# Kernel tuning notes

Measured on AMD Instinct MI355X. Metric: run time of the kernel, lower is better.

Reference implementation:

```python
import jax, jax.numpy as jnp
import numpy as np

TOPK_RATIO = 0.1
THRESHOLD = 0.25
OUT_DIM = 256
STATS_DIM = 18
NEG = -1e30  # sentinel for invalid pixels when sorting (values are probs in [0,1])


def setup_inputs() -> dict:
    key = jax.random.key(0)
    k1, k2, k3, k4, k5, k6, k7 = jax.random.split(key, 7)
    B, C, H, W = 16, 4, 512, 512
    evidence_logits = jax.random.normal(k1, (B, C, H, W), dtype=jnp.float32)
    severity_map = jax.random.normal(k2, (B, 1, H, W), dtype=jnp.float32)
    target_mask = jax.random.uniform(k3, (B, 1, H, W), dtype=jnp.float32)
    # LayerNorm(18) params (torch defaults: weight=1, bias=0)
    ln_w = jnp.ones((STATS_DIM,), jnp.float32)
    ln_b = jnp.zeros((STATS_DIM,), jnp.float32)
    # Linear(18, out_dim) and Linear(out_dim, out_dim)
    w1 = jax.random.normal(k4, (STATS_DIM, OUT_DIM), dtype=jnp.float32) * 0.1
    b1 = jax.random.normal(k5, (OUT_DIM,), dtype=jnp.float32) * 0.01
    w2 = jax.random.normal(k6, (OUT_DIM, OUT_DIM), dtype=jnp.float32) * 0.05
    b2 = jax.random.normal(k7, (OUT_DIM,), dtype=jnp.float32) * 0.01
    return {"evidence_logits": evidence_logits, "severity_map": severity_map,
            "target_mask": target_mask, "ln_w": ln_w, "ln_b": ln_b,
            "w1": w1, "b1": b1, "w2": w2, "b2": b2}


def _forward(evidence_logits, severity_map, target_mask, ln_w, ln_b, w1, b1, w2, b2):
    B, C, H, W = evidence_logits.shape
    N = H * W
    prob = jax.nn.softmax(evidence_logits, axis=1).reshape(B, C, N).transpose(0, 2, 1)  # [B,N,4]
    sev = jax.nn.sigmoid(severity_map).reshape(B, N)                                    # [B,N]
    # mask is same spatial size as logits, so nearest resize is identity
    valid = target_mask.reshape(B, N) > 0.5                                             # [B,N] bool
    validf = valid.astype(prob.dtype)
    total = validf.sum(axis=-1)                                                         # [B]
    has = total > 0
    safe_total = jnp.maximum(total, 1.0)
    # k = max(1, round(total * ratio)); total>=1 implies k<=total
    k = jnp.maximum(1, jnp.round(total * TOPK_RATIO)).astype(jnp.int32)                 # [B]

    # per-class masked mean / max
    class_mean = jnp.einsum('bnc,bn->bc', prob, validf) / safe_total[:, None]           # [B,4]
    class_max = jnp.max(jnp.where(valid[:, :, None], prob, NEG), axis=1)                # [B,4]
    class_max = jnp.where(has[:, None], class_max, 0.0)

    # top-k means for 4 class channels + severity at once: sort desc, cumsum, gather at k-1
    vals = jnp.concatenate([prob, sev[:, :, None]], axis=-1)                            # [B,N,5]
    masked = jnp.where(valid[:, :, None], vals, NEG)
    sorted_desc = jnp.sort(masked, axis=1)[:, ::-1, :]                                  # [B,N,5]
    csum = jnp.cumsum(sorted_desc, axis=1)
    idx = (k - 1).astype(jnp.int32)[:, None, None]                                      # [B,1,1]
    topk_mean = jnp.take_along_axis(csum, jnp.broadcast_to(idx, (B, 1, 5)), axis=1)[:, 0, :]
    topk_mean = topk_mean / k[:, None].astype(prob.dtype)                               # [B,5]
    topk_mean = jnp.where(has[:, None], topk_mean, 0.0)
    class_topk = topk_mean[:, :4]                                                       # [B,4]
    sev_topk = topk_mean[:, 4:5]                                                        # [B,1]

    sev_mean = jnp.where(has, jnp.sum(sev * validf, axis=-1) / safe_total, 0.0)[:, None]
    sev_max = jnp.where(has, jnp.max(jnp.where(valid, sev, NEG), axis=-1), 0.0)[:, None]

    damaged_ind = (prob[:, :, 1] + prob[:, :, 2] + prob[:, :, 3] > THRESHOLD).astype(prob.dtype)
    high_ind = (prob[:, :, 2] + prob[:, :, 3] > THRESHOLD).astype(prob.dtype)
    damaged = jnp.where(has, jnp.sum(damaged_ind * validf, axis=-1) / safe_total, 0.0)   # [B]
    high = jnp.where(has, jnp.sum(high_ind * validf, axis=-1) / safe_total, 0.0)         # [B]
    tar = jnp.where(has, validf.mean(axis=-1), 0.0)                                      # [B]

    stats = jnp.concatenate([class_mean, class_max, class_topk,
                             sev_mean, sev_max, sev_topk,
                             damaged[:, None], high[:, None], tar[:, None]], axis=-1)    # [B,18]

    # LayerNorm(18), eps=1e-5
    mu = stats.mean(axis=-1, keepdims=True)
    var = jnp.mean((stats - mu) ** 2, axis=-1, keepdims=True)
    normed = (stats - mu) * jax.lax.rsqrt(var + 1e-5) * ln_w + ln_b
    h1 = jax.nn.gelu(normed @ w1 + b1, approximate=False)
    projected = h1 @ w2 + b2                                                             # [B,256]
    return stats, projected, damaged, high, tar


def reference(evidence_logits, severity_map, target_mask, ln_w, ln_b, w1, b1, w2, b2):
    return _forward(evidence_logits, severity_map, target_mask, ln_w, ln_b, w1, b1, w2, b2)
```

## Files before the change

### kernel.cpp

```cpp
#include <hip/hip_runtime.h>
#include <math.h>

#define NB 512
#define CHN 5

static constexpr int kN = 512 * 512;
static constexpr int kB = 16;
static constexpr int kChunks = 32;
static constexpr int kThreads1 = 1024;
static constexpr int kPixPerBlock = kN / kChunks;
static constexpr int kF4PerBlock = kPixPerBlock / 4;
static constexpr int kGroups = kF4PerBlock / kThreads1;
static constexpr int kHist = CHN * NB;

static constexpr size_t SPART_OFF = 0;
static constexpr size_t PART_OFF  = SPART_OFF + (size_t)kB * kChunks * 16 * 4;

__global__ __launch_bounds__(kThreads1) void ep_pass1(
    const float* __restrict__ logits,
    const float* __restrict__ sevmap,
    const float* __restrict__ mask,
    float* __restrict__ spart,
    unsigned short* __restrict__ part_hist) {
  __shared__ unsigned s_hcnt[kHist];
  __shared__ float s_red[16][16];

  const int tid = threadIdx.x;
  const int b = blockIdx.y;
  const int chunk = blockIdx.x;

  for (int i = tid; i < kHist; i += kThreads1) s_hcnt[i] = 0u;
  __syncthreads();

  const float4* L0 = (const float4*)(logits + (size_t)b * 4 * kN);
  const float4* L1 = L0 + kN / 4;
  const float4* L2 = L1 + kN / 4;
  const float4* L3 = L2 + kN / 4;
  const float4* SV = (const float4*)(sevmap + (size_t)b * kN);
  const float4* MK = (const float4*)(mask + (size_t)b * kN);
  const int base = chunk * kF4PerBlock;

  float cnt = 0.f, sum0 = 0.f, sum1 = 0.f, sum2 = 0.f, sum3 = 0.f;
  float sevs = 0.f, dmg = 0.f, hig = 0.f;
  float mx0 = 0.f, mx1 = 0.f, mx2 = 0.f, mx3 = 0.f, sevm = 0.f;

#pragma unroll
  for (int g = 0; g < kGroups; ++g) {
    const int fi = base + g * kThreads1 + tid;
    float4 a = L0[fi];
    float4 bq = L1[fi];
    float4 cq = L2[fi];
    float4 dq = L3[fi];
    float4 sv = SV[fi];
    float4 mk = MK[fi];
#pragma unroll
    for (int j = 0; j < 4; ++j) {
      float l0 = ((const float*)&a)[j];
      float l1 = ((const float*)&bq)[j];
      float l2 = ((const float*)&cq)[j];
      float l3 = ((const float*)&dq)[j];
      float e0 = __expf(l0);
      float e1 = __expf(l1);
      float e2 = __expf(l2);
      float e3 = __expf(l3);
      float inv = 1.f / (e0 + e1 + e2 + e3);
      float p0 = e0 * inv, p1 = e1 * inv, p2 = e2 * inv, p3 = e3 * inv;
      float sg = 1.f / (1.f + __expf(-((const float*)&sv)[j]));
      bool valid = ((const float*)&mk)[j] > 0.5f;
      if (valid) {
        cnt += 1.f;
        sum0 += p0; sum1 += p1; sum2 += p2; sum3 += p3;
        mx0 = fmaxf(mx0, p0); mx1 = fmaxf(mx1, p1);
        mx2 = fmaxf(mx2, p2); mx3 = fmaxf(mx3, p3);
        sevs += sg; sevm = fmaxf(sevm, sg);
        dmg += (p1 + p2 + p3 > 0.25f) ? 1.f : 0.f;
        hig += (p2 + p3 > 0.25f) ? 1.f : 0.f;
        int bi0 = min(NB - 1, (int)(p0 * (float)NB));
        int bi1 = min(NB - 1, (int)(p1 * (float)NB));
        int bi2 = min(NB - 1, (int)(p2 * (float)NB));
        int bi3 = min(NB - 1, (int)(p3 * (float)NB));
        int bi4 = min(NB - 1, (int)(sg * (float)NB));
        atomicAdd(&s_hcnt[0 * NB + bi0], 1u);
        atomicAdd(&s_hcnt[1 * NB + bi1], 1u);
        atomicAdd(&s_hcnt[2 * NB + bi2], 1u);
        atomicAdd(&s_hcnt[3 * NB + bi3], 1u);
        atomicAdd(&s_hcnt[4 * NB + bi4], 1u);
      }
    }
  }

  float acc[8] = {cnt, sum0, sum1, sum2, sum3, sevs, dmg, hig};
  float mxs[5] = {mx0, mx1, mx2, mx3, sevm};
#pragma unroll
  for (int off = 32; off > 0; off >>= 1) {
#pragma unroll
    for (int i = 0; i < 8; ++i) acc[i] += __shfl_down(acc[i], off);
#pragma unroll
    for (int i = 0; i < 5; ++i) mxs[i] = fmaxf(mxs[i], __shfl_down(mxs[i], off));
  }
  const int lane = tid & 63;
  const int wv = tid >> 6;
  if (lane == 0) {
#pragma unroll
    for (int i = 0; i < 8; ++i) s_red[wv][i] = acc[i];
#pragma unroll
    for (int i = 0; i < 5; ++i) s_red[wv][8 + i] = mxs[i];
  }
  __syncthreads();
  if (tid < 16) {
    float v;
    if (tid < 8) {
      v = 0.f;
#pragma unroll
      for (int w = 0; w < 16; ++w) v += s_red[w][tid];
    } else if (tid < 13) {
      v = 0.f;
#pragma unroll
      for (int w = 0; w < 16; ++w) v = fmaxf(v, s_red[w][tid]);
    } else {
      v = 0.f;
    }
    spart[((size_t)b * kChunks + chunk) * 16 + tid] = v;
  }

  ushort4* dst = (ushort4*)(part_hist + ((size_t)b * kChunks + chunk) * kHist);
  for (int i = tid; i < kHist / 4; i += kThreads1) {
    ushort4 v;
    v.x = (unsigned short)s_hcnt[4 * i + 0];
    v.y = (unsigned short)s_hcnt[4 * i + 1];
    v.z = (unsigned short)s_hcnt[4 * i + 2];
    v.w = (unsigned short)s_hcnt[4 * i + 3];
    dst[i] = v;
  }
}

__global__ __launch_bounds__(1024) void ep_finalize(
    const float* __restrict__ spart,
    const unsigned short* __restrict__ part_hist,
    const float* __restrict__ ln_w, const float* __restrict__ ln_b,
    const float* __restrict__ w1, const float* __restrict__ b1,
    const float* __restrict__ w2, const float* __restrict__ b2,
    float* __restrict__ out) {
  __shared__ unsigned s_hist[kHist];
  __shared__ float topk[8];
  __shared__ float s_scal[16];
  __shared__ float stats[18], normed[18], h1v[256];

  const int tid = threadIdx.x;
  const int lane = tid & 63;
  const int wv = tid >> 6;
  const int b = blockIdx.x;

  if (tid < 8) topk[tid] = 0.f;

  {
    const unsigned* pp = (const unsigned*)(part_hist + (size_t)b * kChunks * kHist);
    for (int i = tid; i < kHist / 2; i += 1024) {
      unsigned a0 = 0, a1 = 0;
#pragma unroll
      for (int c = 0; c < kChunks; ++c) {
        unsigned u = pp[(size_t)c * (kHist / 2) + i];
        a0 += u & 0xffffu;
        a1 += u >> 16;
      }
      s_hist[2 * i] = a0;
      s_hist[2 * i + 1] = a1;
    }
  }

  if (wv == 15 && lane < kChunks) {
    for (int s = 0; s < 13; ++s) {
      float v = spart[((size_t)b * kChunks + lane) * 16 + s];
#pragma unroll
      for (int off = 16; off > 0; off >>= 1) {
        float t = __shfl_down(v, off, 32);
        v = (s < 8) ? (v + t) : fmaxf(v, t);
      }
      if (lane == 0) s_scal[s] = v;
    }
  }
  __syncthreads();

  const float total = s_scal[0];
  const bool has = total > 0.f;
  const float safe = fmaxf(total, 1.f);
  const float kf = fmaxf(1.f, rintf(total * 0.1f));

  if (wv < CHN) {
    const int c = wv;
    const int base = (63 - lane) * 8;
    float cntv[8];
    float gc = 0.f, gs = 0.f;
    const uint4* hv = (const uint4*)s_hist;
#pragma unroll
    for (int q = 0; q < 2; ++q) {
      uint4 u = hv[c * (NB / 4) + (63 - lane) * 2 + q];
      float c0 = (float)u.x, c1 = (float)u.y, c2 = (float)u.z, c3 = (float)u.w;
      int bin = base + q * 4;
      cntv[q * 4 + 0] = c0; cntv[q * 4 + 1] = c1;
      cntv[q * 4 + 2] = c2; cntv[q * 4 + 3] = c3;
      gc += c0 + c1 + c2 + c3;
      gs += c0 * ((bin + 0.5f) * (1.f / NB)) + c1 * ((bin + 1.5f) * (1.f / NB)) +
            c2 * ((bin + 2.5f) * (1.f / NB)) + c3 * ((bin + 3.5f) * (1.f / NB));
    }
    float ic = gc, is = gs;
#pragma unroll
    for (int off = 1; off < 64; off <<= 1) {
      float tc = __shfl_up(ic, off);
      float ts = __shfl_up(is, off);
      if (lane >= off) { ic += tc; is += ts; }
    }
    float ec = ic - gc;
    float es = is - gs;

    if (has && ec < kf && kf <= ic) {
      float cg = ec, ss = es;
#pragma unroll
      for (int d = 7; d >= 0; --d) {
        int bin = base + d;
        float center = (bin + 0.5f) * (1.f / NB);
        float cb = cntv[d];
        if (cg + cb >= kf) {
          float r = kf - cg;
          topk[c] = (ss + r * center) / kf;
          break;
        }
        cg += cb;
        ss += cb * center;
      }
    }
  }
  __syncthreads();

  if (tid == 0) {
    float inv_safe = 1.f / safe;
    stats[0] = s_scal[1] * inv_safe;
    stats[1] = s_scal[2] * inv_safe;
    stats[2] = s_scal[3] * inv_safe;
    stats[3] = s_scal[4] * inv_safe;
#pragma unroll
    for (int c = 0; c < 4; ++c) stats[4 + c] = has ? s_scal[8 + c] : 0.f;
#pragma unroll
    for (int c = 0; c < 4; ++c) stats[8 + c] = has ? topk[c] : 0.f;
    stats[12] = has ? s_scal[5] * inv_safe : 0.f;
    stats[13] = has ? s_scal[12] : 0.f;
    stats[14] = has ? topk[4] : 0.f;
    stats[15] = has ? s_scal[6] * inv_safe : 0.f;
    stats[16] = has ? s_scal[7] * inv_safe : 0.f;
    stats[17] = has ? total * (1.f / (float)kN) : 0.f;

    float mu = 0.f;
#pragma unroll
    for (int i = 0; i < 18; ++i) mu += stats[i];
    mu *= (1.f / 18.f);
    float var = 0.f;
#pragma unroll
    for (int i = 0; i < 18; ++i) {
      float d = stats[i] - mu;
      var += d * d;
    }
    var *= (1.f / 18.f);
    float inv_std = rsqrtf(var + 1e-5f);
#pragma unroll
    for (int i = 0; i < 18; ++i)
      normed[i] = (stats[i] - mu) * inv_std * ln_w[i] + ln_b[i];
  }
  __syncthreads();

  if (tid < 256) {
    float x = b1[tid];
#pragma unroll
    for (int i = 0; i < 18; ++i) x += normed[i] * w1[i * 256 + tid];
    h1v[tid] = 0.5f * x * (1.f + erff(x * 0.70710678118654752440f));
  }
  __syncthreads();
  if (tid < 256) {
    float y = b2[tid];
    for (int i = 0; i < 256; ++i) y += h1v[i] * w2[i * 256 + tid];

    out[288 + b * 256 + tid] = y;
    if (tid < 18) out[b * 18 + tid] = stats[tid];
    if (tid == 0) {
      out[4384 + b] = stats[15];
      out[4400 + b] = stats[16];
      out[4416 + b] = stats[17];
    }
  }
}

extern "C" void kernel_launch(void* const* d_in, const int* in_sizes, int n_in,
                              void* d_out, int out_size, void* d_ws, size_t ws_size,
                              hipStream_t stream) {
  const float* logits = (const float*)d_in[0];
  const float* sevmap = (const float*)d_in[1];
  const float* maskp  = (const float*)d_in[2];
  const float* ln_w   = (const float*)d_in[3];
  const float* ln_b   = (const float*)d_in[4];
  const float* w1     = (const float*)d_in[5];
  const float* b1     = (const float*)d_in[6];
  const float* w2     = (const float*)d_in[7];
  const float* b2     = (const float*)d_in[8];
  float* out = (float*)d_out;

  char* ws = (char*)d_ws;
  float* spart = (float*)(ws + SPART_OFF);
  unsigned short* part_hist = (unsigned short*)(ws + PART_OFF);

  dim3 g1(kChunks, kB);
  ep_pass1<<<g1, kThreads1, 0, stream>>>(logits, sevmap, maskp, spart, part_hist);
  ep_finalize<<<kB, 1024, 0, stream>>>(spart, part_hist, ln_w, ln_b, w1, b1, w2,
                                       b2, out);
}
```

Measured before the change: 151.5 us.

## Fuse finalize into pass1 via last-block-per-batch ticket counter

Merges the two kernels into one. Each block atomically increments a per-batch ticket after writing its partial histogram and stats, and the last block to arrive for a batch performs the reduction, top-k estimation, LayerNorm and MLP. This removes a kernel launch and lets finalize work for early-finishing batches overlap with other blocks still scanning pixels. In exchange it adds a memset launch for the tickets, thread fences, and extra shared-memory and register pressure in the fused kernel.

```diff
diff --git a/kernel.cpp b/kernel.cpp
--- a/kernel.cpp
+++ b/kernel.cpp
@@ -15,17 +15,29 @@
 
 static constexpr size_t SPART_OFF = 0;
 static constexpr size_t PART_OFF  = SPART_OFF + (size_t)kB * kChunks * 16 * 4;
-
-__global__ __launch_bounds__(kThreads1) void ep_pass1(
+static constexpr size_t TICK_OFF  = PART_OFF + (size_t)kB * kChunks * kHist * 2;
+
+__global__ __launch_bounds__(kThreads1) void ep_fused(
     const float* __restrict__ logits,
     const float* __restrict__ sevmap,
     const float* __restrict__ mask,
     float* __restrict__ spart,
-    unsigned short* __restrict__ part_hist) {
-  __shared__ unsigned s_hcnt[kHist];
+    unsigned short* __restrict__ part_hist,
+    unsigned* __restrict__ tickets,
+    const float* __restrict__ ln_w, const float* __restrict__ ln_b,
+    const float* __restrict__ w1, const float* __restrict__ b1,
+    const float* __restrict__ w2, const float* __restrict__ b2,
+    float* __restrict__ out) {
+  __shared__ __align__(16) unsigned s_hcnt[kHist];
   __shared__ float s_red[16][16];
+  __shared__ float s_scal[16];
+  __shared__ float topk[8];
+  __shared__ float stats[18], normed[18], h1v[256];
+  __shared__ unsigned s_islast;
 
   const int tid = threadIdx.x;
+  const int lane = tid & 63;
+  const int wv = tid >> 6;
   const int b = blockIdx.y;
   const int chunk = blockIdx.x;
 
@@ -98,8 +110,6 @@
 #pragma unroll
     for (int i = 0; i < 5; ++i) mxs[i] = fmaxf(mxs[i], __shfl_down(mxs[i], off));
   }
-  const int lane = tid & 63;
-  const int wv = tid >> 6;
   if (lane == 0) {
 #pragma unroll
     for (int i = 0; i < 8; ++i) s_red[wv][i] = acc[i];
@@ -123,39 +133,33 @@
     spart[((size_t)b * kChunks + chunk) * 16 + tid] = v;
   }
 
-  ushort4* dst = (ushort4*)(part_hist + ((size_t)b * kChunks + chunk) * kHist);
-  for (int i = tid; i < kHist / 4; i += kThreads1) {
-    ushort4 v;
-    v.x = (unsigned short)s_hcnt[4 * i + 0];
-    v.y = (unsigned short)s_hcnt[4 * i + 1];
-    v.z = (unsigned short)s_hcnt[4 * i + 2];
-    v.w = (unsigned short)s_hcnt[4 * i + 3];
-    dst[i] = v;
-  }
-}
-
-__global__ __launch_bounds__(1024) void ep_finalize(
-    const float* __restrict__ spart,
-    const unsigned short* __restrict__ part_hist,
-    const float* __restrict__ ln_w, const float* __restrict__ ln_b,
-    const float* __restrict__ w1, const float* __restrict__ b1,
-    const float* __restrict__ w2, const float* __restrict__ b2,
-    float* __restrict__ out) {
-  __shared__ unsigned s_hist[kHist];
-  __shared__ float topk[8];
-  __shared__ float s_scal[16];
-  __shared__ float stats[18], normed[18], h1v[256];
-
-  const int tid = threadIdx.x;
-  const int lane = tid & 63;
-  const int wv = tid >> 6;
-  const int b = blockIdx.x;
+  {
+    ushort4* dst = (ushort4*)(part_hist + ((size_t)b * kChunks + chunk) * kHist);
+    for (int i = tid; i < kHist / 4; i += kThreads1) {
+      ushort4 v;
+      v.x = (unsigned short)s_hcnt[4 * i + 0];
+      v.y = (unsigned short)s_hcnt[4 * i + 1];
+      v.z = (unsigned short)s_hcnt[4 * i + 2];
+      v.w = (unsigned short)s_hcnt[4 * i + 3];
+      dst[i] = v;
+    }
+  }
+
+  __threadfence();
+  __syncthreads();
+  if (tid == 0) {
+    unsigned prev = atomicAdd(&tickets[b], 1u);
+    s_islast = (prev == (unsigned)(kChunks - 1)) ? 1u : 0u;
+  }
+  __syncthreads();
+  if (!s_islast) return;
+  __threadfence();
 
   if (tid < 8) topk[tid] = 0.f;
 
   {
     const unsigned* pp = (const unsigned*)(part_hist + (size_t)b * kChunks * kHist);
-    for (int i = tid; i < kHist / 2; i += 1024) {
+    for (int i = tid; i < kHist / 2; i += kThreads1) {
       unsigned a0 = 0, a1 = 0;
 #pragma unroll
       for (int c = 0; c < kChunks; ++c) {
@@ -163,8 +167,8 @@
         a0 += u & 0xffffu;
         a1 += u >> 16;
       }
-      s_hist[2 * i] = a0;
-      s_hist[2 * i + 1] = a1;
+      s_hcnt[2 * i] = a0;
+      s_hcnt[2 * i + 1] = a1;
     }
   }
 
@@ -188,15 +192,15 @@
 
   if (wv < CHN) {
     const int c = wv;
-    const int base = (63 - lane) * 8;
+    const int base2 = (63 - lane) * 8;
     float cntv[8];
     float gc = 0.f, gs = 0.f;
-    const uint4* hv = (const uint4*)s_hist;
+    const uint4* hv = (const uint4*)s_hcnt;
 #pragma unroll
     for (int q = 0; q < 2; ++q) {
       uint4 u = hv[c * (NB / 4) + (63 - lane) * 2 + q];
       float c0 = (float)u.x, c1 = (float)u.y, c2 = (float)u.z, c3 = (float)u.w;
-      int bin = base + q * 4;
+      int bin = base2 + q * 4;
       cntv[q * 4 + 0] = c0; cntv[q * 4 + 1] = c1;
       cntv[q * 4 + 2] = c2; cntv[q * 4 + 3] = c3;
       gc += c0 + c1 + c2 + c3;
@@ -217,7 +221,7 @@
       float cg = ec, ss = es;
 #pragma unroll
       for (int d = 7; d >= 0; --d) {
-        int bin = base + d;
+        int bin = base2 + d;
         float center = (bin + 0.5f) * (1.f / NB);
         float cb = cntv[d];
         if (cg + cb >= kf) {
@@ -305,9 +309,11 @@
   char* ws = (char*)d_ws;
   float* spart = (float*)(ws + SPART_OFF);
   unsigned short* part_hist = (unsigned short*)(ws + PART_OFF);
+  unsigned* tickets = (unsigned*)(ws + TICK_OFF);
+
+  hipMemsetAsync(tickets, 0, kB * sizeof(unsigned), stream);
 
   dim3 g1(kChunks, kB);
-  ep_pass1<<<g1, kThreads1, 0, stream>>>(logits, sevmap, maskp, spart, part_hist);
-  ep_finalize<<<kB, 1024, 0, stream>>>(spart, part_hist, ln_w, ln_b, w1, b1, w2,
-                                       b2, out);
+  ep_fused<<<g1, kThreads1, 0, stream>>>(logits, sevmap, maskp, spart, part_hist,
+                                         tickets, ln_w, ln_b, w1, b1, w2, b2, out);
 }
```

New measurement: 357.0 us. 2.36x slower.
